# Optimization experiments

Hardware: AMD Instinct MI355X
Metric: run time of the kernel (lower is better)

## Reference

```python
import jax, jax.numpy as jnp
import numpy as np

ALPHA = 0.2  # LeakyReLU negative slope
NEG_BIG = -9e15

def setup_inputs() -> dict:
    key = jax.random.key(0)
    k1, k2, k3, k4 = jax.random.split(key, 4)
    N, F_IN, F_OUT = 8192, 128, 128
    h = jax.random.normal(k1, (N, F_IN), dtype=jnp.float32)
    adj = jax.random.randint(k2, (N, N), 0, 2, dtype=jnp.int32)
    # xavier-uniform-ish params
    W = jax.random.normal(k3, (F_IN, F_OUT), dtype=jnp.float32) * (1.0 / np.sqrt(F_IN))
    a = jax.random.normal(k4, (2 * F_OUT, 1), dtype=jnp.float32) * (1.0 / np.sqrt(2 * F_OUT))
    return {"h": h, "adj": adj, "W": W, "a": a}

def reference(h, adj, W, a):
    # Wh: [N, F_OUT]
    Wh = h @ W
    F_out = Wh.shape[1]
    # a_input @ a == (Wh @ a1)_i + (Wh @ a2)_j  (same math, no N^2*2F tensor)
    a1 = a[:F_out, 0]   # [F_OUT]
    a2 = a[F_out:, 0]   # [F_OUT]
    e = (Wh @ a1)[:, None] + (Wh @ a2)[None, :]        # [N, N]
    e = jnp.where(e >= 0, e, ALPHA * e)                # LeakyReLU(0.2)
    scores = jnp.where(adj > 0, e, NEG_BIG)
    attention = jax.nn.softmax(scores, axis=1)         # row-wise
    # dropout skipped (eval mode / training=False)
    return attention @ Wh                              # [N, F_OUT]
```

## Files before the change

### kernel.cpp

```cpp
#include <hip/hip_runtime.h>
#include <hip/hip_bf16.h>

#define N 8192
#define FD 128
#define LOG2E 1.4426950408889634f

typedef __attribute__((ext_vector_type(4))) float f4;
typedef __attribute__((ext_vector_type(4))) int i32x4;
typedef __attribute__((ext_vector_type(4))) unsigned int u32x4;
typedef __attribute__((ext_vector_type(8))) __bf16 bf16x8;

__device__ __forceinline__ unsigned short bfbits(float x){
  __bf16 b = (__bf16)x;
  return __builtin_bit_cast(unsigned short, b);
}

__global__ __launch_bounds__(256) void k12_wh(const float* __restrict__ h,
                                              const float* __restrict__ W,
                                              const float* __restrict__ a,
                                              unsigned short* __restrict__ Bsw,
                                              float* __restrict__ s1L,
                                              float* __restrict__ s2L){
  __shared__ float Wl[64*128];
  __shared__ float hT[128*33];
  int t = threadIdx.x;
  int i0 = blockIdx.x * 32;
  {
    int r  = t >> 3;
    int k0 = (t & 7) * 16;
    const f4* src = (const f4*)&h[(size_t)(i0 + r)*FD + k0];
    #pragma unroll
    for (int q = 0; q < 4; ++q){
      f4 v = src[q];
      #pragma unroll
      for (int e = 0; e < 4; ++e) hT[(k0 + q*4 + e)*33 + r] = v[e];
    }
  }
  int f0 = (t & 31) * 4;
  int r0 = (t >> 5) * 4;
  float acc[4][4] = {};
  for (int half = 0; half < 2; ++half){
    __syncthreads();
    #pragma unroll
    for (int v = 0; v < 8; ++v){
      int idx = (v*256 + t)*4;
      *(f4*)&Wl[idx] = *(const f4*)&W[half*8192 + idx];
    }
    __syncthreads();
    for (int k2 = 0; k2 < 64; ++k2){
      f4 wv = *(const f4*)&Wl[k2*FD + f0];
      f4 hv = *(const f4*)&hT[(half*64 + k2)*33 + r0];
      #pragma unroll
      for (int ri = 0; ri < 4; ++ri)
        #pragma unroll
        for (int fi = 0; fi < 4; ++fi)
          acc[ri][fi] = __builtin_fmaf(hv[ri], wv[fi], acc[ri][fi]);
    }
  }
  int jblk = blockIdx.x;
  int n  = f0 >> 4;
  int fl = f0 & 15;
  #pragma unroll
  for (int ri = 0; ri < 4; ++ri){
    int k = r0 + ri;
    size_t base = (((size_t)jblk*8 + n)*64 + ((k>>3)<<4))*8 + (k&7);
    #pragma unroll
    for (int fi = 0; fi < 4; ++fi)
      Bsw[base + (size_t)(fl + fi)*8] = bfbits(acc[ri][fi]);
  }
  f4 a1v = *(const f4*)&a[f0];
  f4 a2v = *(const f4*)&a[FD + f0];
  float p1[4], p2[4];
  #pragma unroll
  for (int ri = 0; ri < 4; ++ri){
    p1[ri] = 0.f; p2[ri] = 0.f;
    #pragma unroll
    for (int fi = 0; fi < 4; ++fi){
      p1[ri] = __builtin_fmaf(acc[ri][fi], a1v[fi], p1[ri]);
      p2[ri] = __builtin_fmaf(acc[ri][fi], a2v[fi], p2[ri]);
    }
  }
  #pragma unroll
  for (int d = 1; d < 32; d <<= 1){
    #pragma unroll
    for (int ri = 0; ri < 4; ++ri){
      p1[ri] += __shfl_xor(p1[ri], d, 32);
      p2[ri] += __shfl_xor(p2[ri], d, 32);
    }
  }
  if ((t & 31) == 0){
    #pragma unroll
    for (int ri = 0; ri < 4; ++ri){
      s1L[i0 + r0 + ri] = p1[ri] * LOG2E;
      s2L[i0 + r0 + ri] = p2[ri] * LOG2E;
    }
  }
}

__global__ __launch_bounds__(256) void k3_max(const float* __restrict__ s2L,
                                              float* __restrict__ M2L){
  __shared__ float red[4];
  int t = threadIdx.x;
  float m = -3.0e38f;
  for (int i = t; i < N; i += 256) m = fmaxf(m, s2L[i]);
  #pragma unroll
  for (int d = 1; d < 64; d <<= 1) m = fmaxf(m, __shfl_xor(m, d, 64));
  if ((t & 63) == 0) red[t >> 6] = m;
  __syncthreads();
  if (t == 0) *M2L = fmaxf(fmaxf(red[0], red[1]), fmaxf(red[2], red[3]));
}

__global__ __launch_bounds__(256,4) void k4_flash(const int* __restrict__ adj,
    const unsigned short* __restrict__ Bsw,
    const float* __restrict__ s1L, const float* __restrict__ s2L,
    const float* __restrict__ M2p,
    float* __restrict__ partial, float* __restrict__ denomp, int njc){
  __shared__ __align__(16) unsigned char bswl[32768];
  __shared__ __align__(16) unsigned char mknib[128*32];
  __shared__ __align__(16) float s2l[128];
  int t = threadIdx.x;
  int wv = t >> 6, lane = t & 63;
  int lrow = lane & 15, lgrp = lane >> 4;
  int bx = blockIdx.x;
  int jlen = N / njc;
  int jstart = blockIdx.y * jlen;
  int nmac = jlen >> 7;
  float M2 = *M2p;
  int i0w = bx*128 + wv*32;
  float s1a = s1L[i0w + lrow], s1b = s1L[i0w + 16 + lrow];
  float ea = s1a + M2, eb = s1b + M2;
  float maL = fmaxf(ea, 0.2f*ea);
  float mbL = fmaxf(eb, 0.2f*eb);

  f4 acc[2][8]; f4 accd[2];
  #pragma unroll
  for (int x = 0; x < 2; ++x){
    accd[x] = (f4){0.f,0.f,0.f,0.f};
    #pragma unroll
    for (int n = 0; n < 8; ++n) acc[x][n] = (f4){0.f,0.f,0.f,0.f};
  }
  u32x4 onesbits = (u32x4){0x3F803F80u,0x3F803F80u,0x3F803F80u,0x3F803F80u};
  bf16x8 ones = __builtin_bit_cast(bf16x8, onesbits);

  const i32x4* adj4 = (const i32x4*)adj;
  int sr2 = lane >> 5;
  int sj  = lane & 31;
  size_t abase = ((size_t)(bx*128 + wv*32 + sr2) * N) >> 2;

  for (int m = 0; m < nmac; ++m){
    int jb0 = jstart + m*128;
    const unsigned int* bg = (const unsigned int*)(Bsw + (size_t)(jb0 >> 5) * 4096);
    #pragma unroll
    for (int q = 0; q < 8; ++q){
      int chunk = q*4 + wv;
      __builtin_amdgcn_global_load_lds(
        (const __attribute__((address_space(1))) unsigned int*)(bg + (size_t)(chunk*64 + lane)*4),
        (__attribute__((address_space(3))) unsigned int*)(bswl + chunk*1024),
        16, 0, 0);
    }
    size_t ab = abase + (size_t)(jb0 >> 2) + sj;
    #pragma unroll
    for (int eb = 0; eb < 4; ++eb){
      i32x4 st[4];
      #pragma unroll
      for (int e = 0; e < 4; ++e)
        st[e] = adj4[ab + (size_t)(eb*4 + e) * 4096];
      #pragma unroll
      for (int e = 0; e < 4; ++e){
        unsigned nib = (st[e][0] != 0 ? 1u : 0u) | (st[e][1] != 0 ? 2u : 0u)
                     | (st[e][2] != 0 ? 4u : 0u) | (st[e][3] != 0 ? 8u : 0u);
        int rloc = wv*32 + (eb*4 + e)*2 + sr2;
        mknib[rloc*32 + sj] = (unsigned char)nib;
      }
    }
    if (t < 32) *(f4*)&s2l[t*4] = *(const f4*)&s2L[jb0 + t*4];
    __syncthreads();
    #pragma unroll
    for (int js = 0; js < 4; ++js){
      int jo = js*32 + lgrp*8;
      f4 ya = *(const f4*)&s2l[jo];
      f4 yb = *(const f4*)&s2l[jo+4];
      int gb = (js*4 + lgrp)*2;
      unsigned short ua = *(const unsigned short*)&mknib[(wv*32 + lrow)*32 + gb];
      unsigned short ub = *(const unsigned short*)&mknib[(wv*32 + 16 + lrow)*32 + gb];
      unsigned mba = (ua & 0xFu) | ((ua >> 4) & 0xF0u);
      unsigned mbb = (ub & 0xFu) | ((ub >> 4) & 0xF0u);
      bf16x8 fa, fb;
      #pragma unroll
      for (int e = 0; e < 8; ++e){
        float sjv = (e < 4) ? ya[e] : yb[e-4];
        float xa = s1a + sjv,            xb = s1b + sjv;
        float la = fmaxf(xa, 0.2f*xa),   lb = fmaxf(xb, 0.2f*xb);
        float pa = ((mba>>e)&1u) ? __builtin_amdgcn_exp2f(la - maL) : 0.f;
        float pb = ((mbb>>e)&1u) ? __builtin_amdgcn_exp2f(lb - mbL) : 0.f;
        fa[e] = (__bf16)pa; fb[e] = (__bf16)pb;
      }
      accd[0] = __builtin_amdgcn_mfma_f32_16x16x32_bf16(fa, ones, accd[0], 0, 0, 0);
      accd[1] = __builtin_amdgcn_mfma_f32_16x16x32_bf16(fb, ones, accd[1], 0, 0, 0);
      {
        u32x4 b0[4];
        #pragma unroll
        for (int n = 0; n < 4; ++n)
          b0[n] = *(const u32x4*)&bswl[((js*8 + n)*64 + lane)*16];
        #pragma unroll
        for (int n = 0; n < 4; ++n){
          bf16x8 bb = __builtin_bit_cast(bf16x8, b0[n]);
          acc[0][n] = __builtin_amdgcn_mfma_f32_16x16x32_bf16(fa, bb, acc[0][n], 0, 0, 0);
          acc[1][n] = __builtin_amdgcn_mfma_f32_16x16x32_bf16(fb, bb, acc[1][n], 0, 0, 0);
        }
      }
      {
        u32x4 b1[4];
        #pragma unroll
        for (int n = 0; n < 4; ++n)
          b1[n] = *(const u32x4*)&bswl[((js*8 + 4 + n)*64 + lane)*16];
        #pragma unroll
        for (int n = 0; n < 4; ++n){
          bf16x8 bb = __builtin_bit_cast(bf16x8, b1[n]);
          acc[0][4+n] = __builtin_amdgcn_mfma_f32_16x16x32_bf16(fa, bb, acc[0][4+n], 0, 0, 0);
          acc[1][4+n] = __builtin_amdgcn_mfma_f32_16x16x32_bf16(fb, bb, acc[1][4+n], 0, 0, 0);
        }
      }
    }
    __syncthreads();
  }

  if (lrow == 0){
    #pragma unroll
    for (int x = 0; x < 2; ++x)
      #pragma unroll
      for (int r = 0; r < 4; ++r)
        denomp[(size_t)blockIdx.y*N + i0w + x*16 + lgrp*4 + r] = accd[x][r];
  }
  float* pb = partial + (size_t)blockIdx.y * N * FD;
  #pragma unroll
  for (int x = 0; x < 2; ++x)
    #pragma unroll
    for (int n = 0; n < 8; ++n)
      #pragma unroll
      for (int r = 0; r < 4; ++r)
        pb[(size_t)(i0w + x*16 + lgrp*4 + r)*FD + n*16 + lrow] = acc[x][n][r];
}

__global__ __launch_bounds__(256) void k5_fin(const float* __restrict__ partial,
    const float* __restrict__ denomp, float* __restrict__ out, int njc){
  int g = blockIdx.x*256 + threadIdx.x;
  int i = g >> 7;
  float num = 0.f, den = 0.f;
  for (int c = 0; c < njc; ++c) num += partial[(size_t)c*N*FD + g];
  for (int c = 0; c < njc; ++c) den += denomp[(size_t)c*N + i];
  out[g] = num / den;
}

extern "C" void kernel_launch(void* const* d_in, const int* in_sizes, int n_in,
                              void* d_out, int out_size, void* d_ws, size_t ws_size,
                              hipStream_t stream){
  const float* h   = (const float*)d_in[0];
  const int*   adj = (const int*)d_in[1];
  const float* W   = (const float*)d_in[2];
  const float* a   = (const float*)d_in[3];
  float* out = (float*)d_out;
  char* ws = (char*)d_ws;

  unsigned short* Bsw = (unsigned short*)ws;
  float* s1L = (float*)(ws + (size_t)(6u<<20));
  float* s2L = (float*)(ws + (size_t)(6u<<20) + 32768);
  float* M2L = (float*)(ws + (size_t)(6u<<20) + 65536);
  float* denomp  = (float*)(ws + (size_t)(7u<<20));
  float* partial = (float*)(ws + (size_t)(8u<<20));

  size_t chunk = (size_t)N * FD * sizeof(float);
  int njc = 1;
  if (ws_size > ((size_t)(8u<<20))){
    size_t m = (ws_size - (size_t)(8u<<20)) / chunk;
    njc = (m >= 16) ? 16 : (m >= 8) ? 8 : (m >= 4) ? 4 : (m >= 2) ? 2 : 1;
  }

  hipLaunchKernelGGL(k12_wh, dim3(256), dim3(256), 0, stream, h, W, a, Bsw, s1L, s2L);
  hipLaunchKernelGGL(k3_max, dim3(1),   dim3(256), 0, stream, s2L, M2L);
  hipLaunchKernelGGL(k4_flash, dim3(64, njc), dim3(256), 0, stream,
                     adj, Bsw, s1L, s2L, M2L, partial, denomp, njc);
  hipLaunchKernelGGL(k5_fin, dim3(N*FD/256), dim3(256), 0, stream, partial, denomp, out, njc);
}
```

Before: 437.0 us.

## Double-buffer LDS tiles and prefetch adjacency in the flash attention loop

Double-buffers the Bsw tile, mask nibbles and s2 values in shared memory. The next tile's LDS loads and 16 adjacency vector loads are issued before the MFMA work on the current tile, and mask packing happens after it. This hides global load latency behind compute and halves the barriers per iteration. It also lowers occupancy hints from 4 to 2 blocks per CU, flattens the grid so blocks sharing the same rows launch next to each other (which may help cache reuse), and caps the j-split at 8. The cost is doubled LDS use, more registers held by the prefetched adjacency, and a smaller split count, which leaves fewer blocks in flight.

```diff
diff --git a/kernel.cpp b/kernel.cpp
--- a/kernel.cpp
+++ b/kernel.cpp
@@ -110,20 +110,22 @@
   if (t == 0) *M2L = fmaxf(fmaxf(red[0], red[1]), fmaxf(red[2], red[3]));
 }
 
-__global__ __launch_bounds__(256,4) void k4_flash(const int* __restrict__ adj,
+__global__ __launch_bounds__(256,2) void k4_flash(const int* __restrict__ adj,
     const unsigned short* __restrict__ Bsw,
     const float* __restrict__ s1L, const float* __restrict__ s2L,
     const float* __restrict__ M2p,
     float* __restrict__ partial, float* __restrict__ denomp, int njc){
-  __shared__ __align__(16) unsigned char bswl[32768];
-  __shared__ __align__(16) unsigned char mknib[128*32];
-  __shared__ __align__(16) float s2l[128];
+  __shared__ __align__(16) unsigned char bswl[2][32768];
+  __shared__ __align__(16) unsigned char mknib[2][128*32];
+  __shared__ __align__(16) float s2l[2][128];
   int t = threadIdx.x;
   int wv = t >> 6, lane = t & 63;
   int lrow = lane & 15, lgrp = lane >> 4;
-  int bx = blockIdx.x;
+  int bid = blockIdx.x;
+  int y  = bid & (njc - 1);
+  int bx = bid / njc;
   int jlen = N / njc;
-  int jstart = blockIdx.y * jlen;
+  int jstart = y * jlen;
   int nmac = jlen >> 7;
   float M2 = *M2p;
   int i0w = bx*128 + wv*32;
@@ -147,42 +149,57 @@
   int sj  = lane & 31;
   size_t abase = ((size_t)(bx*128 + wv*32 + sr2) * N) >> 2;
 
+  i32x4 st[16];
+
+  #define STAGE_BSW(jb0, b) do {                                               \
+    const unsigned int* bg = (const unsigned int*)(Bsw + (size_t)((jb0) >> 5) * 4096); \
+    _Pragma("unroll")                                                          \
+    for (int q = 0; q < 8; ++q){                                               \
+      int chunk = q*4 + wv;                                                    \
+      __builtin_amdgcn_global_load_lds(                                        \
+        (const __attribute__((address_space(1))) unsigned int*)(bg + (size_t)(chunk*64 + lane)*4), \
+        (__attribute__((address_space(3))) unsigned int*)(&bswl[b][0] + chunk*1024), \
+        16, 0, 0);                                                             \
+    }                                                                          \
+  } while(0)
+
+  #define STAGE_ADJ(jb0) do {                                                  \
+    size_t ab = abase + (size_t)((jb0) >> 2) + sj;                             \
+    _Pragma("unroll")                                                          \
+    for (int e = 0; e < 16; ++e) st[e] = adj4[ab + (size_t)e * 4096];          \
+  } while(0)
+
+  #define PACK_MASKS(b) do {                                                   \
+    _Pragma("unroll")                                                          \
+    for (int e = 0; e < 16; ++e){                                              \
+      unsigned nib = (st[e][0] != 0 ? 1u : 0u) | (st[e][1] != 0 ? 2u : 0u)     \
+                   | (st[e][2] != 0 ? 4u : 0u) | (st[e][3] != 0 ? 8u : 0u);    \
+      int rloc = wv*32 + e*2 + sr2;                                            \
+      mknib[b][rloc*32 + sj] = (unsigned char)nib;                             \
+    }                                                                          \
+  } while(0)
+
+  int buf = 0;
+  STAGE_BSW(jstart, 0);
+  STAGE_ADJ(jstart);
+  PACK_MASKS(0);
+  if (t < 32) *(f4*)&s2l[0][t*4] = *(const f4*)&s2L[jstart + t*4];
+  __syncthreads();
+
   for (int m = 0; m < nmac; ++m){
     int jb0 = jstart + m*128;
-    const unsigned int* bg = (const unsigned int*)(Bsw + (size_t)(jb0 >> 5) * 4096);
-    #pragma unroll
-    for (int q = 0; q < 8; ++q){
-      int chunk = q*4 + wv;
-      __builtin_amdgcn_global_load_lds(
-        (const __attribute__((address_space(1))) unsigned int*)(bg + (size_t)(chunk*64 + lane)*4),
-        (__attribute__((address_space(3))) unsigned int*)(bswl + chunk*1024),
-        16, 0, 0);
-    }
-    size_t ab = abase + (size_t)(jb0 >> 2) + sj;
-    #pragma unroll
-    for (int eb = 0; eb < 4; ++eb){
-      i32x4 st[4];
-      #pragma unroll
-      for (int e = 0; e < 4; ++e)
-        st[e] = adj4[ab + (size_t)(eb*4 + e) * 4096];
-      #pragma unroll
-      for (int e = 0; e < 4; ++e){
-        unsigned nib = (st[e][0] != 0 ? 1u : 0u) | (st[e][1] != 0 ? 2u : 0u)
-                     | (st[e][2] != 0 ? 4u : 0u) | (st[e][3] != 0 ? 8u : 0u);
-        int rloc = wv*32 + (eb*4 + e)*2 + sr2;
-        mknib[rloc*32 + sj] = (unsigned char)nib;
-      }
-    }
-    if (t < 32) *(f4*)&s2l[t*4] = *(const f4*)&s2L[jb0 + t*4];
-    __syncthreads();
+    if (m + 1 < nmac){
+      STAGE_BSW(jb0 + 128, buf ^ 1);
+      STAGE_ADJ(jb0 + 128);
+    }
     #pragma unroll
     for (int js = 0; js < 4; ++js){
       int jo = js*32 + lgrp*8;
-      f4 ya = *(const f4*)&s2l[jo];
-      f4 yb = *(const f4*)&s2l[jo+4];
+      f4 ya = *(const f4*)&s2l[buf][jo];
+      f4 yb = *(const f4*)&s2l[buf][jo+4];
       int gb = (js*4 + lgrp)*2;
-      unsigned short ua = *(const unsigned short*)&mknib[(wv*32 + lrow)*32 + gb];
-      unsigned short ub = *(const unsigned short*)&mknib[(wv*32 + 16 + lrow)*32 + gb];
+      unsigned short ua = *(const unsigned short*)&mknib[buf][(wv*32 + lrow)*32 + gb];
+      unsigned short ub = *(const unsigned short*)&mknib[buf][(wv*32 + 16 + lrow)*32 + gb];
       unsigned mba = (ua & 0xFu) | ((ua >> 4) & 0xF0u);
       unsigned mbb = (ub & 0xFu) | ((ub >> 4) & 0xF0u);
       bf16x8 fa, fb;
@@ -201,7 +218,7 @@
         u32x4 b0[4];
         #pragma unroll
         for (int n = 0; n < 4; ++n)
-          b0[n] = *(const u32x4*)&bswl[((js*8 + n)*64 + lane)*16];
+          b0[n] = *(const u32x4*)&bswl[buf][((js*8 + n)*64 + lane)*16];
         #pragma unroll
         for (int n = 0; n < 4; ++n){
           bf16x8 bb = __builtin_bit_cast(bf16x8, b0[n]);
@@ -213,7 +230,7 @@
         u32x4 b1[4];
         #pragma unroll
         for (int n = 0; n < 4; ++n)
-          b1[n] = *(const u32x4*)&bswl[((js*8 + 4 + n)*64 + lane)*16];
+          b1[n] = *(const u32x4*)&bswl[buf][((js*8 + 4 + n)*64 + lane)*16];
         #pragma unroll
         for (int n = 0; n < 4; ++n){
           bf16x8 bb = __builtin_bit_cast(bf16x8, b1[n]);
@@ -222,7 +239,12 @@
         }
       }
     }
+    if (m + 1 < nmac){
+      PACK_MASKS(buf ^ 1);
+      if (t < 32) *(f4*)&s2l[buf ^ 1][t*4] = *(const f4*)&s2L[jb0 + 128 + t*4];
+    }
     __syncthreads();
+    buf ^= 1;
   }
 
   if (lrow == 0){
@@ -230,9 +252,9 @@
     for (int x = 0; x < 2; ++x)
       #pragma unroll
       for (int r = 0; r < 4; ++r)
-        denomp[(size_t)blockIdx.y*N + i0w + x*16 + lgrp*4 + r] = accd[x][r];
-  }
-  float* pb = partial + (size_t)blockIdx.y * N * FD;
+        denomp[(size_t)y*N + i0w + x*16 + lgrp*4 + r] = accd[x][r];
+  }
+  float* pb = partial + (size_t)y * N * FD;
   #pragma unroll
   for (int x = 0; x < 2; ++x)
     #pragma unroll
@@ -273,12 +295,12 @@
   int njc = 1;
   if (ws_size > ((size_t)(8u<<20))){
     size_t m = (ws_size - (size_t)(8u<<20)) / chunk;
-    njc = (m >= 16) ? 16 : (m >= 8) ? 8 : (m >= 4) ? 4 : (m >= 2) ? 2 : 1;
+    njc = (m >= 8) ? 8 : (m >= 4) ? 4 : (m >= 2) ? 2 : 1;
   }
 
   hipLaunchKernelGGL(k12_wh, dim3(256), dim3(256), 0, stream, h, W, a, Bsw, s1L, s2L);
   hipLaunchKernelGGL(k3_max, dim3(1),   dim3(256), 0, stream, s2L, M2L);
-  hipLaunchKernelGGL(k4_flash, dim3(64, njc), dim3(256), 0, stream,
+  hipLaunchKernelGGL(k4_flash, dim3(64*njc), dim3(256), 0, stream,
                      adj, Bsw, s1L, s2L, M2L, partial, denomp, njc);
   hipLaunchKernelGGL(k5_fin, dim3(N*FD/256), dim3(256), 0, stream, partial, denomp, out, njc);
 }
```

Measured after the change: 402.3 us. -7.9%, faster.
